# Kernel optimization log

Hardware: AMD Instinct MI355X
Metric: run time of the kernel (lower is better)

## Reference

```python
import jax, jax.numpy as jnp
import numpy as np

NPOINT = 2048
NSAMPLE = 16
LEAKY = 0.1
BN_EPS = 1e-5


def square_distance(src, dst):
    # src [B,S,3], dst [B,N,3] -> [B,S,N] squared euclidean
    d = -2.0 * jnp.einsum('bsc,bnc->bsn', src, dst)
    d = d + jnp.sum(src * src, -1)[:, :, None]
    d = d + jnp.sum(dst * dst, -1)[:, None, :]
    return d


def furthest_point_sample(xyz, npoint):
    # xyz [B,N,3] -> idx [B,npoint]; matches pointnet2 CUDA (seed = index 0)
    B, N, _ = xyz.shape

    def step(carry, _):
        dist, far = carry  # dist [B,N], far [B]
        centroid = jnp.take_along_axis(xyz, far[:, None, None], axis=1)  # [B,1,3]
        d = jnp.sum((xyz - centroid) ** 2, axis=-1)
        dist = jnp.minimum(dist, d)
        nxt = jnp.argmax(dist, axis=-1).astype(jnp.int32)
        return (dist, nxt), far

    init = (jnp.full((B, N), 1e10, xyz.dtype), jnp.zeros((B,), jnp.int32))
    _, idxs = jax.lax.scan(step, init, None, length=npoint)
    return idxs.T  # [B, npoint]


def _gather_nbrs(p, i):
    # p [N,C], i [S,K] -> [S,K,C]
    return p[i]


gather_group = jax.vmap(_gather_nbrs)


def conv_bn_lrelu(x, W, g, b):
    # x [B,Cin,S,K], W [Cout,Cin]; 1x1 conv + train-mode BatchNorm2d + LeakyReLU
    y = jnp.einsum('oc,bcsk->bosk', W, x)
    mean = jnp.mean(y, axis=(0, 2, 3), keepdims=True)
    var = jnp.var(y, axis=(0, 2, 3), keepdims=True)
    y = (y - mean) * jax.lax.rsqrt(var + BN_EPS)
    y = y * g[None, :, None, None] + b[None, :, None, None]
    return jnp.where(y > 0, y, LEAKY * y)


def setup_inputs() -> dict:
    key = jax.random.key(0)
    ks = jax.random.split(key, 5)
    B, N, D = 4, 8192, 64
    return {
        'xyz': jax.random.normal(ks[0], (B, 3, N), jnp.float32),
        'points': jax.random.normal(ks[1], (B, D, N), jnp.float32),
        'conv0_w': jax.random.normal(ks[2], (64, 67), jnp.float32) * 0.05,
        'conv1_w': jax.random.normal(ks[3], (64, 64), jnp.float32) * 0.05,
        'conv2_w': jax.random.normal(ks[4], (128, 64), jnp.float32) * 0.05,
        'bn0_g': jnp.ones((64,), jnp.float32),
        'bn0_b': jnp.zeros((64,), jnp.float32),
        'bn1_g': jnp.ones((64,), jnp.float32),
        'bn1_b': jnp.zeros((64,), jnp.float32),
        'bn2_g': jnp.ones((128,), jnp.float32),
        'bn2_b': jnp.zeros((128,), jnp.float32),
    }


def reference(xyz, points, conv0_w, conv1_w, conv2_w,
              bn0_g, bn0_b, bn1_g, bn1_b, bn2_g, bn2_b):
    xyz_t = jnp.transpose(xyz, (0, 2, 1))      # [B,N,3]
    pts_t = jnp.transpose(points, (0, 2, 1))   # [B,N,D]

    fps_idx = furthest_point_sample(xyz_t, NPOINT)                       # [B,S]
    new_xyz = jnp.take_along_axis(xyz_t, fps_idx[:, :, None], axis=1)    # [B,S,3]

    sqrd = square_distance(new_xyz, xyz_t)                               # [B,S,N]
    _, idx = jax.lax.top_k(-sqrd, NSAMPLE)                               # [B,S,K]

    grouped_xyz = gather_group(xyz_t, idx)                               # [B,S,K,3]
    grouped_norm = grouped_xyz - new_xyz[:, :, None, :]
    grouped_pts = gather_group(pts_t, idx)                               # [B,S,K,D]
    new_points = jnp.concatenate([grouped_norm, grouped_pts], axis=-1)   # [B,S,K,D+3]
    new_points = jnp.transpose(new_points, (0, 3, 1, 2))                 # [B,D+3,S,K]

    for W, g, b in ((conv0_w, bn0_g, bn0_b), (conv1_w, bn1_g, bn1_b),
                    (conv2_w, bn2_g, bn2_b)):
        new_points = conv_bn_lrelu(new_points, W, g, b)

    feat = jnp.max(new_points, axis=-1)                                  # [B,128,S]
    return jnp.transpose(new_xyz, (0, 2, 1)), feat, fps_idx
```

## Files before the change

### kernel.cpp

```cpp
#include <hip/hip_runtime.h>
#include <hip/hip_bf16.h>

#define BB 4
#define NP 8192
#define SS 2048
#define KK 16
#define DD 64
#define NN (BB*SS*KK)
#define HEATERS 128

typedef float vf2 __attribute__((ext_vector_type(2)));

__device__ __forceinline__ float wave_prefix_max_f32(float v) {
  int x;
  x = __builtin_amdgcn_update_dpp(0, __float_as_int(v), 0xB1, 0xF, 0xF, true);
  v = fmaxf(v, __int_as_float(x));
  x = __builtin_amdgcn_update_dpp(0, __float_as_int(v), 0x4E, 0xF, 0xF, true);
  v = fmaxf(v, __int_as_float(x));
  x = __builtin_amdgcn_update_dpp(0, __float_as_int(v), 0x141, 0xF, 0xF, true);
  v = fmaxf(v, __int_as_float(x));
  x = __builtin_amdgcn_update_dpp(0, __float_as_int(v), 0x140, 0xF, 0xF, true);
  v = fmaxf(v, __int_as_float(x));
  x = __builtin_amdgcn_update_dpp(0, __float_as_int(v), 0x142, 0xF, 0xF, true);
  v = fmaxf(v, __int_as_float(x));
  x = __builtin_amdgcn_update_dpp(0, __float_as_int(v), 0x143, 0xF, 0xF, true);
  v = fmaxf(v, __int_as_float(x));
  return v;
}

__global__ __launch_bounds__(512) void fps_kernel(
    const float* __restrict__ xyz, float* __restrict__ newXyz,
    float* __restrict__ out, int* __restrict__ done)
{
  const int t = threadIdx.x;

  if (blockIdx.x >= BB) {
    float a0 = 1.0f, a1 = 1.1f, a2 = 1.2f, a3 = 1.3f;
    const float bm = 1.000001f, cm = 1e-7f;
    for (;;) {
      for (int k = 0; k < 1024; k++) {
        a0 = __builtin_fmaf(a0, bm, cm);
        a1 = __builtin_fmaf(a1, bm, cm);
        a2 = __builtin_fmaf(a2, bm, cm);
        a3 = __builtin_fmaf(a3, bm, cm);
      }
      if (__hip_atomic_load(done, __ATOMIC_RELAXED, __HIP_MEMORY_SCOPE_AGENT) >= BB)
        break;
    }
    if (a0 == 123.456f && a1 == 2.f && a2 == 3.f && a3 == 4.f)
      ((volatile int*)done)[1] = 1;
    return;
  }

  const int b = blockIdx.x;
  const float* xb = xyz + (size_t)b * 3 * NP;

  __shared__ float lx[NP], ly[NP], lz[NP];
  __shared__ int   wis[SS];
  __shared__ unsigned long long swin[3];

  vf2 px[8], py[8], pz[8], dist[8];
  const int i0 = t << 4;
#pragma unroll
  for (int h = 0; h < 8; h++) {
    int i = i0 + (h << 1);
    vf2 x = *(const vf2*)(xb + i);
    vf2 y = *(const vf2*)(xb + NP + i);
    vf2 z = *(const vf2*)(xb + 2 * NP + i);
    px[h] = x; py[h] = y; pz[h] = z;
    dist[h] = (vf2){1e10f, 1e10f};
    *(vf2*)(lx + i) = x; *(vf2*)(ly + i) = y; *(vf2*)(lz + i) = z;
  }
  if (t == 0) { wis[0] = 0; swin[0] = 0; swin[1] = 0; swin[2] = 0; }
  __syncthreads();

  float cx = lx[0], cy = ly[0], cz = lz[0];

  for (int it = 1; it < SS; ++it) {
    vf2 c2x = {cx, cx}, c2y = {cy, cy}, c2z = {cz, cz};
    vf2 lb = {-1.0f, -1.0f};
    {
#pragma clang fp contract(off)
#pragma unroll
      for (int h = 0; h < 8; h++) {
        vf2 dx = px[h] - c2x;
        vf2 dy = py[h] - c2y;
        vf2 dz = pz[h] - c2z;
        vf2 d  = (dx * dx + dy * dy) + dz * dz;
        vf2 dm = __builtin_elementwise_min(dist[h], d);
        dist[h] = dm;
        lb = __builtin_elementwise_max(lb, dm);
      }
    }
    float lbest = fmaxf(lb.x, lb.y);
    float Vp = wave_prefix_max_f32(lbest);
    int q = it % 3;
    if (lbest == Vp) {
      unsigned mi = 0u;
#pragma unroll
      for (int h = 7; h >= 0; h--) {
        unsigned base = (unsigned)(i0 + (h << 1));
        if (dist[h].y == lbest) mi = base + 1;
        if (dist[h].x == lbest) mi = base;
      }
      unsigned long long pk =
          ((unsigned long long)__float_as_uint(lbest) << 32) | (unsigned)(~mi);
      atomicMax(&swin[q], pk);
    }
    __syncthreads();
    unsigned long long pkf = swin[q];
    int ii = (int)(~((unsigned)pkf));
    if (t == 0) { wis[it] = ii; swin[(q + 2) % 3] = 0; }
    cx = lx[ii]; cy = ly[ii]; cz = lz[ii];
  }
  __syncthreads();

  float* outX = out;
  float* outI = out + 24576 + 1048576;
  for (int s = t; s < SS; s += 512) {
    int iw = wis[s];
    float x = lx[iw], y = ly[iw], z = lz[iw];
    size_t qq = (size_t)(b * SS + s);
    newXyz[qq * 3 + 0] = x;
    newXyz[qq * 3 + 1] = y;
    newXyz[qq * 3 + 2] = z;
    outX[(b * 3 + 0) * SS + s] = x;
    outX[(b * 3 + 1) * SS + s] = y;
    outX[(b * 3 + 2) * SS + s] = z;
    outI[b * SS + s] = (float)iw;
  }
  if (t == 0)
    __hip_atomic_fetch_add(done, 1, __ATOMIC_RELEASE, __HIP_MEMORY_SCOPE_AGENT);
}

__global__ __launch_bounds__(256) void knn_kernel(
    const float* __restrict__ xyz, const float* __restrict__ newXyz,
    int* __restrict__ knnIdx)
{
  const int t = threadIdx.x, w = t >> 6, l = t & 63;
  const int q = blockIdx.x * 4 + w;
  const int b = q >> 11;
  const float* xb = xyz + (size_t)b * 3 * NP;
  float qx = newXyz[q * 3], qy = newXyz[q * 3 + 1], qz = newXyz[q * 3 + 2];
  float ss = __fadd_rn(__fadd_rn(__fmul_rn(qx, qx), __fmul_rn(qy, qy)), __fmul_rn(qz, qz));
  float kd[16]; int ki[16];
#pragma unroll
  for (int j = 0; j < 16; j++) { kd[j] = __builtin_inff(); ki[j] = 0x7fffffff; }

  for (int m = 0; m < 128; m++) {
    int i = l + (m << 6);
    float x = xb[i], y = xb[NP + i], z = xb[2 * NP + i];
    float dot = __fadd_rn(__fadd_rn(__fmul_rn(x, qx), __fmul_rn(y, qy)), __fmul_rn(z, qz));
    float nn  = __fadd_rn(__fadd_rn(__fmul_rn(x, x), __fmul_rn(y, y)), __fmul_rn(z, z));
    float d   = __fadd_rn(__fadd_rn(__fmul_rn(-2.0f, dot), ss), nn);
    if (d < kd[15]) {
      kd[15] = d; ki[15] = i;
#pragma unroll
      for (int jj = 15; jj >= 1; jj--) {
        if (kd[jj] < kd[jj - 1]) {
          float td = kd[jj]; kd[jj] = kd[jj - 1]; kd[jj - 1] = td;
          int   ti = ki[jj]; ki[jj] = ki[jj - 1]; ki[jj - 1] = ti;
        }
      }
    }
  }

  __shared__ float sd[4 * 64 * 17];
  __shared__ int   sx[4 * 64 * 17];
  int base = (w * 64 + l) * 17;
#pragma unroll
  for (int j = 0; j < 16; j++) { sd[base + j] = kd[j]; sx[base + j] = ki[j]; }
  __syncthreads();

  int cur = 0; int outIdx = 0;
#pragma unroll 1
  for (int r = 0; r < 16; r++) {
    float hv = (cur < 16) ? sd[base + cur] : __builtin_inff();
    int   hi = (cur < 16) ? sx[base + cur] : 0x7fffffff;
    int   hl = l;
#pragma unroll
    for (int m2 = 1; m2 < 64; m2 <<= 1) {
      float ov = __shfl_xor(hv, m2, 64);
      int   oi = __shfl_xor(hi, m2, 64);
      int   ol = __shfl_xor(hl, m2, 64);
      if (ov < hv || (ov == hv && oi < hi)) { hv = ov; hi = oi; hl = ol; }
    }
    if (l == hl) cur++;
    if (l == r) outIdx = hi;
  }
  if (l < 16) knnIdx[q * 16 + l] = outIdx;
}

__global__ __launch_bounds__(256, 2) void conv0_kernel(
    const float* __restrict__ xyz, const float* __restrict__ points,
    const float* __restrict__ newXyz, const int* __restrict__ knnIdx,
    const float* __restrict__ W, float* __restrict__ Y)
{
  int n = blockIdx.x * 256 + threadIdx.x;
  int b = n >> 15;
  int q = n >> 4;
  int ip = knnIdx[n];
  const float* xb = xyz + (size_t)b * 3 * NP;
  float x[67];
  x[0] = xb[ip]          - newXyz[q * 3 + 0];
  x[1] = xb[NP + ip]     - newXyz[q * 3 + 1];
  x[2] = xb[2 * NP + ip] - newXyz[q * 3 + 2];
  const float* pb = points + (size_t)b * DD * NP + ip;
#pragma unroll 8
  for (int d0 = 0; d0 < DD; d0++) x[3 + d0] = pb[(size_t)d0 * NP];

#pragma unroll 1
  for (int o = 0; o < 64; o += 4) {
    float a0 = 0.f, a1 = 0.f, a2 = 0.f, a3 = 0.f;
#pragma unroll
    for (int c = 0; c < 67; c++) {
      float xv = x[c];
      a0 = fmaf(W[(o + 0) * 67 + c], xv, a0);
      a1 = fmaf(W[(o + 1) * 67 + c], xv, a1);
      a2 = fmaf(W[(o + 2) * 67 + c], xv, a2);
      a3 = fmaf(W[(o + 3) * 67 + c], xv, a3);
    }
    Y[(size_t)(o + 0) * NN + n] = a0;
    Y[(size_t)(o + 1) * NN + n] = a1;
    Y[(size_t)(o + 2) * NN + n] = a2;
    Y[(size_t)(o + 3) * NN + n] = a3;
  }
}

template <int CIN, int COUT>
__global__ __launch_bounds__(256, 2) void conv_kernel(
    const float* __restrict__ X, const float* __restrict__ W,
    const float* __restrict__ stats, const float* __restrict__ g,
    const float* __restrict__ bt, float* __restrict__ Y)
{
  __shared__ vf2 sss[CIN];
  for (int i = threadIdx.x; i < CIN; i += 256) {
    float mean = stats[2 * i] * (1.0f / NN);
    float var  = stats[2 * i + 1] * (1.0f / NN) - mean * mean;
    float inv  = rsqrtf(var + 1e-5f);
    float sc = inv * g[i];
    float sh = bt[i] - mean * sc;
    sss[i] = (vf2){sc, sh};
  }
  __syncthreads();

  int n = blockIdx.x * 256 + threadIdx.x;
  float x[CIN];
#pragma unroll
  for (int c = 0; c < CIN; c++) x[c] = X[(size_t)c * NN + n];
#pragma unroll
  for (int c = 0; c < CIN; c++) {
    vf2 p = sss[c];
    float v = fmaf(x[c], p.x, p.y);
    x[c] = v > 0.0f ? v : 0.1f * v;
  }
#pragma unroll 1
  for (int o = 0; o < COUT; o += 4) {
    float a0 = 0.f, a1 = 0.f, a2 = 0.f, a3 = 0.f;
#pragma unroll
    for (int c = 0; c < CIN; c++) {
      float xv = x[c];
      a0 = fmaf(W[(o + 0) * CIN + c], xv, a0);
      a1 = fmaf(W[(o + 1) * CIN + c], xv, a1);
      a2 = fmaf(W[(o + 2) * CIN + c], xv, a2);
      a3 = fmaf(W[(o + 3) * CIN + c], xv, a3);
    }
    Y[(size_t)(o + 0) * NN + n] = a0;
    Y[(size_t)(o + 1) * NN + n] = a1;
    Y[(size_t)(o + 2) * NN + n] = a2;
    Y[(size_t)(o + 3) * NN + n] = a3;
  }
}

__global__ __launch_bounds__(256) void stats_kernel(
    const float* __restrict__ Y, float* __restrict__ stats)
{
  int c = blockIdx.y;
  int base = blockIdx.x * 4096 + threadIdx.x;
  const float* yc = Y + (size_t)c * NN;
  float s1 = 0.f, s2 = 0.f;
#pragma unroll
  for (int j = 0; j < 16; j++) {
    float v = yc[base + j * 256];
    s1 += v; s2 = fmaf(v, v, s2);
  }
#pragma unroll
  for (int m = 1; m < 64; m <<= 1) {
    s1 += __shfl_xor(s1, m, 64);
    s2 += __shfl_xor(s2, m, 64);
  }
  __shared__ float r1[4], r2[4];
  int w = threadIdx.x >> 6;
  if ((threadIdx.x & 63) == 0) { r1[w] = s1; r2[w] = s2; }
  __syncthreads();
  if (threadIdx.x == 0) {
    float t1 = r1[0] + r1[1] + r1[2] + r1[3];
    float t2 = r2[0] + r2[1] + r2[2] + r2[3];
    atomicAdd(&stats[c * 2], t1);
    atomicAdd(&stats[c * 2 + 1], t2);
  }
}

__global__ __launch_bounds__(256) void maxk_kernel(
    const float* __restrict__ X, const float* __restrict__ stats,
    const float* __restrict__ g, const float* __restrict__ bt,
    float* __restrict__ out)
{
  int m = blockIdx.x * 256 + threadIdx.x;
  int s = m & 2047;
  int o = (m >> 11) & 127;
  int b = m >> 18;
  float mean = stats[2 * o] * (1.0f / NN);
  float var  = stats[2 * o + 1] * (1.0f / NN) - mean * mean;
  float inv  = rsqrtf(var + 1e-5f);
  float sc = inv * g[o];
  float sh = bt[o] - mean * sc;
  const float4* p = (const float4*)(X + (size_t)o * NN + ((size_t)((b << 11) + s) << 4));
  float mx = -__builtin_inff();
#pragma unroll
  for (int j = 0; j < 4; j++) {
    float4 v4 = p[j];
    float a = fmaf(v4.x, sc, sh); a = a > 0.f ? a : 0.1f * a;
    float b2 = fmaf(v4.y, sc, sh); b2 = b2 > 0.f ? b2 : 0.1f * b2;
    float c = fmaf(v4.z, sc, sh); c = c > 0.f ? c : 0.1f * c;
    float d = fmaf(v4.w, sc, sh); d = d > 0.f ? d : 0.1f * d;
    mx = fmaxf(mx, fmaxf(fmaxf(a, b2), fmaxf(c, d)));
  }
  out[24576 + (size_t)((b << 7) + o) * SS + s] = mx;
}

extern "C" void kernel_launch(void* const* d_in, const int* in_sizes, int n_in,
                              void* d_out, int out_size, void* d_ws, size_t ws_size,
                              hipStream_t stream) {
  const float* xyz    = (const float*)d_in[0];
  const float* points = (const float*)d_in[1];
  const float* w0 = (const float*)d_in[2];
  const float* w1 = (const float*)d_in[3];
  const float* w2 = (const float*)d_in[4];
  const float* g0 = (const float*)d_in[5];
  const float* b0 = (const float*)d_in[6];
  const float* g1 = (const float*)d_in[7];
  const float* b1 = (const float*)d_in[8];
  const float* g2 = (const float*)d_in[9];
  const float* b2 = (const float*)d_in[10];
  float* out = (float*)d_out;

  float* wsf    = (float*)d_ws;
  float* newXyz = wsf;
  int*   knnIdx = (int*)(wsf + 24576);
  float* stats0 = wsf + 155648;
  float* stats1 = wsf + 155904;
  float* stats2 = wsf + 156160;
  int*   done   = (int*)(wsf + 157440);
  float* Xa     = wsf + 160000;
  float* Xb     = wsf + 8941824;

  hipMemsetAsync(stats0, 0, 2048 * 4, stream);

  fps_kernel<<<BB + HEATERS, 512, 0, stream>>>(xyz, newXyz, out, done);
  knn_kernel<<<SS * BB / 4, 256, 0, stream>>>(xyz, newXyz, knnIdx);

  conv0_kernel<<<NN / 256, 256, 0, stream>>>(xyz, points, newXyz, knnIdx, w0, Xb);
  stats_kernel<<<dim3(32, 64), 256, 0, stream>>>(Xb, stats0);

  conv_kernel<64, 64><<<NN / 256, 256, 0, stream>>>(Xb, w1, stats0, g0, b0, Xa);
  stats_kernel<<<dim3(32, 64), 256, 0, stream>>>(Xa, stats1);

  conv_kernel<64, 128><<<NN / 256, 256, 0, stream>>>(Xa, w2, stats1, g1, b1, Xb);
  stats_kernel<<<dim3(32, 128), 256, 0, stream>>>(Xb, stats2);

  maxk_kernel<<<(BB * 128 * SS) / 256, 256, 0, stream>>>(Xb, stats2, g2, b2, out);
}
```

Measured before the change: 2.459 ms.

## Prune FPS distance updates with Morton-sorted point ownership and bounding spheres

Points are bucketed into an 8x8x8 Morton grid, counting-sorted in shared memory, and each thread is assigned 16 spatially clustered points with a bounding sphere. In each FPS iteration a thread skips its distance update when the triangle inequality shows the new centroid cannot reduce any of its current minimum distances. Argmax tie-breaking maps back to the original indices so results match. The aim is to cut per-iteration ALU work, at the cost of extra setup (atomics, a prefix scan, more shared memory and registers). It also adds branching that only saves time when every lane in a wave skips, while the loop stays bound by its per-iteration barrier.

```diff
diff --git a/kernel.cpp b/kernel.cpp
--- a/kernel.cpp
+++ b/kernel.cpp
@@ -26,6 +26,13 @@
   x = __builtin_amdgcn_update_dpp(0, __float_as_int(v), 0x143, 0xF, 0xF, true);
   v = fmaxf(v, __int_as_float(x));
   return v;
+}
+
+__device__ __forceinline__ int morton3(int x, int y, int z) {
+  int m = (x & 1) | ((y & 1) << 1) | ((z & 1) << 2);
+  m |= ((x & 2) << 2) | ((y & 2) << 3) | ((z & 2) << 4);
+  m |= ((x & 4) << 4) | ((y & 4) << 5) | ((z & 4) << 6);
+  return m;
 }
 
 __global__ __launch_bounds__(512) void fps_kernel(
@@ -58,50 +65,130 @@
   __shared__ float lx[NP], ly[NP], lz[NP];
   __shared__ int   wis[SS];
   __shared__ unsigned long long swin[3];
-
+  __shared__ unsigned scnt[512];
+  __shared__ int   sidx[NP];
+
+  const int i0 = t << 4;
+
+  int mycell[16];
+  if (t < 512) scnt[t] = 0;
+  {
+    vf2 xr[8], yr[8], zr[8];
+#pragma unroll
+    for (int h = 0; h < 8; h++) {
+      int i = i0 + (h << 1);
+      xr[h] = *(const vf2*)(xb + i);
+      yr[h] = *(const vf2*)(xb + NP + i);
+      zr[h] = *(const vf2*)(xb + 2 * NP + i);
+      *(vf2*)(lx + i) = xr[h]; *(vf2*)(ly + i) = yr[h]; *(vf2*)(lz + i) = zr[h];
+    }
+    __syncthreads();
+#pragma unroll
+    for (int h = 0; h < 8; h++) {
+      float xs[2] = {xr[h].x, xr[h].y};
+      float ys[2] = {yr[h].x, yr[h].y};
+      float zs[2] = {zr[h].x, zr[h].y};
+#pragma unroll
+      for (int u = 0; u < 2; u++) {
+        int cxg = min(7, max(0, (int)((xs[u] + 5.0f) * 0.8f)));
+        int cyg = min(7, max(0, (int)((ys[u] + 5.0f) * 0.8f)));
+        int czg = min(7, max(0, (int)((zs[u] + 5.0f) * 0.8f)));
+        int c = morton3(cxg, cyg, czg);
+        mycell[(h << 1) + u] = c;
+        atomicAdd(&scnt[c], 1u);
+      }
+    }
+  }
+  __syncthreads();
+
+  unsigned mycnt = scnt[t];
+  for (int s = 1; s < 512; s <<= 1) {
+    unsigned v = (t >= s) ? scnt[t - s] : 0u;
+    __syncthreads();
+    scnt[t] += v;
+    __syncthreads();
+  }
+  unsigned excl = scnt[t] - mycnt;
+  __syncthreads();
+  scnt[t] = excl;
+  __syncthreads();
+
+#pragma unroll
+  for (int j = 0; j < 16; j++) {
+    unsigned pos = atomicAdd(&scnt[mycell[j]], 1u);
+    sidx[pos] = i0 + j;
+  }
+  __syncthreads();
+
+  int oidx[16];
   vf2 px[8], py[8], pz[8], dist[8];
-  const int i0 = t << 4;
-#pragma unroll
-  for (int h = 0; h < 8; h++) {
-    int i = i0 + (h << 1);
-    vf2 x = *(const vf2*)(xb + i);
-    vf2 y = *(const vf2*)(xb + NP + i);
-    vf2 z = *(const vf2*)(xb + 2 * NP + i);
-    px[h] = x; py[h] = y; pz[h] = z;
-    dist[h] = (vf2){1e10f, 1e10f};
-    *(vf2*)(lx + i) = x; *(vf2*)(ly + i) = y; *(vf2*)(lz + i) = z;
+  float bcx, bcy, bcz, r_safe;
+  {
+    float sx = 0.f, sy = 0.f, sz = 0.f;
+#pragma unroll
+    for (int h = 0; h < 16; h++) {
+      int o = sidx[i0 + h];
+      oidx[h] = o;
+      float x = lx[o], y = ly[o], z = lz[o];
+      ((float*)px)[h] = x; ((float*)py)[h] = y; ((float*)pz)[h] = z;
+      sx += x; sy += y; sz += z;
+    }
+    bcx = sx * 0.0625f; bcy = sy * 0.0625f; bcz = sz * 0.0625f;
+    float r2 = 0.f;
+#pragma unroll
+    for (int h = 0; h < 16; h++) {
+      float dx = ((float*)px)[h] - bcx;
+      float dy = ((float*)py)[h] - bcy;
+      float dz = ((float*)pz)[h] - bcz;
+      r2 = fmaxf(r2, dx * dx + dy * dy + dz * dz);
+    }
+    r_safe = sqrtf(r2) * 1.001f + 1e-5f;
+#pragma unroll
+    for (int h = 0; h < 8; h++) dist[h] = (vf2){1e10f, 1e10f};
   }
   if (t == 0) { wis[0] = 0; swin[0] = 0; swin[1] = 0; swin[2] = 0; }
   __syncthreads();
 
   float cx = lx[0], cy = ly[0], cz = lz[0];
+  float lmax = 1e10f;
+  float thr2;
+  { float s = sqrtf(lmax) * 1.001f + r_safe; thr2 = s * s * 1.0001f + 1e-5f; }
 
   for (int it = 1; it < SS; ++it) {
-    vf2 c2x = {cx, cx}, c2y = {cy, cy}, c2z = {cz, cz};
-    vf2 lb = {-1.0f, -1.0f};
-    {
+    float dxc = cx - bcx, dyc = cy - bcy, dzc = cz - bcz;
+    float d2cb = dxc * dxc + dyc * dyc + dzc * dzc;
+    float lbest;
+    if (d2cb <= thr2) {
+      vf2 c2x = {cx, cx}, c2y = {cy, cy}, c2z = {cz, cz};
+      vf2 lb = {-1.0f, -1.0f};
+      {
 #pragma clang fp contract(off)
 #pragma unroll
-      for (int h = 0; h < 8; h++) {
-        vf2 dx = px[h] - c2x;
-        vf2 dy = py[h] - c2y;
-        vf2 dz = pz[h] - c2z;
-        vf2 d  = (dx * dx + dy * dy) + dz * dz;
-        vf2 dm = __builtin_elementwise_min(dist[h], d);
-        dist[h] = dm;
-        lb = __builtin_elementwise_max(lb, dm);
+        for (int h = 0; h < 8; h++) {
+          vf2 dx = px[h] - c2x;
+          vf2 dy = py[h] - c2y;
+          vf2 dz = pz[h] - c2z;
+          vf2 d  = (dx * dx + dy * dy) + dz * dz;
+          vf2 dm = __builtin_elementwise_min(dist[h], d);
+          dist[h] = dm;
+          lb = __builtin_elementwise_max(lb, dm);
+        }
       }
-    }
-    float lbest = fmaxf(lb.x, lb.y);
+      lbest = fmaxf(lb.x, lb.y);
+      lmax = lbest;
+      float s = sqrtf(lbest) * 1.001f + r_safe;
+      thr2 = s * s * 1.0001f + 1e-5f;
+    } else {
+      lbest = lmax;
+    }
     float Vp = wave_prefix_max_f32(lbest);
     int q = it % 3;
     if (lbest == Vp) {
-      unsigned mi = 0u;
-#pragma unroll
-      for (int h = 7; h >= 0; h--) {
-        unsigned base = (unsigned)(i0 + (h << 1));
-        if (dist[h].y == lbest) mi = base + 1;
-        if (dist[h].x == lbest) mi = base;
+      unsigned mi = 0xFFFFFFFFu;
+#pragma unroll
+      for (int h = 0; h < 8; h++) {
+        if (dist[h].x == lbest) mi = min(mi, (unsigned)oidx[(h << 1)]);
+        if (dist[h].y == lbest) mi = min(mi, (unsigned)oidx[(h << 1) + 1]);
       }
       unsigned long long pk =
           ((unsigned long long)__float_as_uint(lbest) << 32) | (unsigned)(~mi);
```

Measured after the change: 2.692 ms. +9.5%, slower.
